# Kernel optimization log

Measured on AMD Instinct MI355X. Metric: run time of the kernel, lower is better.

The kernel has to match this reference:

```python
import jax, jax.numpy as jnp
import numpy as np

H = 1024      # hidden_dim
NH = 16       # num_heads
HD = H // NH  # head_dim
FFN = 4096
EPS = 1e-5


def setup_inputs() -> dict:
    key = jax.random.key(0)
    ks = jax.random.split(key, 12)
    s = 0.02
    return {
        "x": jax.random.normal(ks[0], (2, 2048, H), dtype=jnp.float32),
        "w_qkv": jax.random.normal(ks[1], (H, 3 * H), dtype=jnp.float32) * s,
        "b_qkv": jnp.zeros((3 * H,), dtype=jnp.float32),
        "w_out": jax.random.normal(ks[2], (H, H), dtype=jnp.float32) * s,
        "b_out": jnp.zeros((H,), dtype=jnp.float32),
        "ln1_g": jnp.ones((H,), dtype=jnp.float32),
        "ln1_b": jnp.zeros((H,), dtype=jnp.float32),
        "ln2_g": jnp.ones((H,), dtype=jnp.float32),
        "ln2_b": jnp.zeros((H,), dtype=jnp.float32),
        "w1": jax.random.normal(ks[3], (H, FFN), dtype=jnp.float32) * s,
        "b1": jnp.zeros((FFN,), dtype=jnp.float32),
        "w2": jax.random.normal(ks[4], (FFN, H), dtype=jnp.float32) * s,
        "b2": jnp.zeros((H,), dtype=jnp.float32),
    }


def _layernorm(x, g, b):
    mu = jnp.mean(x, axis=-1, keepdims=True)
    var = jnp.mean(jnp.square(x - mu), axis=-1, keepdims=True)
    return (x - mu) * jax.lax.rsqrt(var + EPS) * g + b


def reference(x, w_qkv, b_qkv, w_out, b_out, ln1_g, ln1_b, ln2_g, ln2_b, w1, b1, w2, b2):
    B, S, _ = x.shape
    # pre-LN attention branch
    h = _layernorm(x, ln1_g, ln1_b)
    qkv = h @ w_qkv + b_qkv                       # (B,S,3H)
    qkv = qkv.reshape(B, S, 3, NH, HD).transpose(2, 0, 3, 1, 4)
    q, k, v = qkv[0], qkv[1], qkv[2]              # (B,NH,S,HD)
    scores = jnp.einsum("bhqd,bhkd->bhqk", q, k) / jnp.sqrt(jnp.float32(HD))
    causal = jnp.triu(jnp.ones((S, S), dtype=bool), k=1)
    scores = jnp.where(causal, -jnp.inf, scores)
    attn = jax.nn.softmax(scores, axis=-1)
    out = jnp.einsum("bhqk,bhkd->bhqd", attn, v)  # (B,NH,S,HD)
    out = out.transpose(0, 2, 1, 3).reshape(B, S, H)
    attn_out = out @ w_out + b_out
    x = x + attn_out
    # FFN branch
    h2 = _layernorm(x, ln2_g, ln2_b)
    ffn = jax.nn.gelu(h2 @ w1 + b1, approximate=False) @ w2 + b2
    return x + ffn
```

## Files before the change

kernel.cpp:

```cpp
#include <hip/hip_runtime.h>
#include <hip/hip_bf16.h>

typedef __bf16 bf16_t;
typedef __bf16 bf16x8 __attribute__((ext_vector_type(8)));
typedef __bf16 bf16x4 __attribute__((ext_vector_type(4)));
typedef __bf16 bf16x2 __attribute__((ext_vector_type(2)));
typedef float  f32x4  __attribute__((ext_vector_type(4)));

#define HDIM 1024
#define SEQ  2048
#define NHEAD 16
#define HEADD 64

__device__ __forceinline__ void gld_lds16(const void* g, void* l) {
  __builtin_amdgcn_global_load_lds(
      (const __attribute__((address_space(1))) unsigned int*)g,
      (__attribute__((address_space(3))) unsigned int*)l, 16, 0, 0);
}

__global__ __launch_bounds__(256) void ln_kernel(const float* __restrict__ x,
                                                 const float* __restrict__ gam,
                                                 const float* __restrict__ bet,
                                                 bf16_t* __restrict__ out) {
  int row = blockIdx.x;
  int t = threadIdx.x;
  const float4* xr = (const float4*)(x + (size_t)row * HDIM);
  float4 v = xr[t];
  float s = v.x + v.y + v.z + v.w;
  float ss = v.x*v.x + v.y*v.y + v.z*v.z + v.w*v.w;
  #pragma unroll
  for (int o = 32; o > 0; o >>= 1) {
    s  += __shfl_xor(s, o);
    ss += __shfl_xor(ss, o);
  }
  __shared__ float red[8];
  int w = t >> 6;
  if ((t & 63) == 0) { red[w*2] = s; red[w*2+1] = ss; }
  __syncthreads();
  s  = red[0] + red[2] + red[4] + red[6];
  ss = red[1] + red[3] + red[5] + red[7];
  float mu  = s * (1.0f / HDIM);
  float var = ss * (1.0f / HDIM) - mu * mu;
  float rstd = rsqrtf(var + 1e-5f);
  float4 g4 = ((const float4*)gam)[t];
  float4 b4 = ((const float4*)bet)[t];
  bf16x4 o4;
  o4[0] = (bf16_t)((v.x - mu) * rstd * g4.x + b4.x);
  o4[1] = (bf16_t)((v.y - mu) * rstd * g4.y + b4.y);
  o4[2] = (bf16_t)((v.z - mu) * rstd * g4.z + b4.z);
  o4[3] = (bf16_t)((v.w - mu) * rstd * g4.w + b4.w);
  *(bf16x4*)(out + (size_t)row * HDIM + t * 4) = o4;
}

__global__ __launch_bounds__(256) void transpose_cast(const float* __restrict__ W,
                                                      bf16_t* __restrict__ Wt,
                                                      int Kd, int Nd) {
  __shared__ float tile[32][33];
  int n0 = blockIdx.x * 32, k0 = blockIdx.y * 32;
  int tx = threadIdx.x & 31, ty = threadIdx.x >> 5;
  #pragma unroll
  for (int i = 0; i < 4; i++)
    tile[ty + i*8][tx] = W[(size_t)(k0 + ty + i*8) * Nd + n0 + tx];
  __syncthreads();
  #pragma unroll
  for (int i = 0; i < 4; i++)
    Wt[(size_t)(n0 + ty + i*8) * Kd + k0 + tx] = (bf16_t)tile[tx][ty + i*8];
}

__device__ __forceinline__ float gelu_fast(float x) {
  float y = 0.7978845608f * (x + 0.044715f * x * x * x);
  float u = exp2f(y * 2.885390082f);
  float th = 1.0f - 2.0f * __builtin_amdgcn_rcpf(u + 1.0f);
  return 0.5f * x * (1.0f + th);
}

template<int EPI, int BN, int BK>
__global__ __launch_bounds__(256, 2)
void gemm_bt(const bf16_t* __restrict__ A, const bf16_t* __restrict__ Bt,
             const float* __restrict__ bias, const float* __restrict__ resid,
             void* __restrict__ outp, int M, int N, int K) {
  constexpr int NFRAG = BN / 32;
  constexpr int CH  = BK / 8;
  constexpr int SWZ = CH - 1;
  constexpr int RPP = 256 / CH;
  __shared__ bf16_t As[2][128*BK];
  __shared__ bf16_t Bs[2][BN*BK];
  int t = threadIdx.x;
  int w = t >> 6, l = t & 63;
  int wr = w >> 1, wc = w & 1;

  int nbx = gridDim.x;
  int bid = blockIdx.y * nbx + blockIdx.x;
  int chunkx = (nbx * gridDim.y) >> 3;
  int nb = (bid & 7) * chunkx + (bid >> 3);
  int bm = nb / nbx, bn = nb % nbx;
  size_t m0 = (size_t)bm * 128, n0 = (size_t)bn * BN;

  f32x4 acc[4][NFRAG];
  #pragma unroll
  for (int m = 0; m < 4; m++)
    #pragma unroll
    for (int n = 0; n < NFRAG; n++) acc[m][n] = (f32x4)(0.0f);

  int srow = t / CH;
  int scol = ((t & SWZ) ^ (srow & SWZ)) * 8;
  int dsto = t * 8;
  const bf16_t* ag = A  + (m0 + srow) * K + scol;
  const bf16_t* bg = Bt + (n0 + srow) * K + scol;

  int lr = l & 15, lg = l >> 4;

  auto stage = [&](int buf, int k0) {
    #pragma unroll
    for (int p = 0; p < 128/RPP; p++)
      gld_lds16(ag + k0 + (size_t)(p*RPP)*K, &As[buf][dsto + p*RPP*BK]);
    #pragma unroll
    for (int p = 0; p < BN/RPP; p++)
      gld_lds16(bg + k0 + (size_t)(p*RPP)*K, &Bs[buf][dsto + p*RPP*BK]);
  };

  stage(0, 0);
  __syncthreads();
  int cur = 0;
  for (int k0 = 0; k0 < K; k0 += BK) {
    if (k0 + BK < K) stage(cur ^ 1, k0 + BK);
    #pragma unroll
    for (int kk = 0; kk < BK/32; kk++) {
      bf16x8 af[4], bfr[NFRAG];
      #pragma unroll
      for (int m = 0; m < 4; m++) {
        int row = wr*64 + m*16 + lr;
        int off = row*BK*2 + (((kk*4 + lg) ^ (row & SWZ)) << 4);
        af[m] = *(const bf16x8*)((const char*)&As[cur][0] + off);
      }
      #pragma unroll
      for (int n = 0; n < NFRAG; n++) {
        int row = wc*(BN/2) + n*16 + lr;
        int off = row*BK*2 + (((kk*4 + lg) ^ (row & SWZ)) << 4);
        bfr[n] = *(const bf16x8*)((const char*)&Bs[cur][0] + off);
      }
      #pragma unroll
      for (int m = 0; m < 4; m++)
        #pragma unroll
        for (int n = 0; n < NFRAG; n++)
          acc[m][n] = __builtin_amdgcn_mfma_f32_16x16x32_bf16(af[m], bfr[n], acc[m][n], 0, 0, 0);
    }
    __syncthreads();
    cur ^= 1;
  }

  int r0 = (l >> 4) * 4, c0 = l & 15;
  #pragma unroll
  for (int m = 0; m < 4; m++) {
    #pragma unroll
    for (int n = 0; n < NFRAG; n++) {
      size_t row = m0 + wr*64 + m*16 + r0;
      size_t col = n0 + wc*(BN/2) + n*16 + c0;
      float bv = bias[col];
      #pragma unroll
      for (int r = 0; r < 4; r++) {
        float vv = acc[m][n][r] + bv;
        size_t idx = (row + r) * (size_t)N + col;
        if (EPI == 0) {
          ((bf16_t*)outp)[idx] = (bf16_t)vv;
        } else if (EPI == 1) {
          ((float*)outp)[idx] = vv + resid[idx];
        } else {
          ((bf16_t*)outp)[idx] = (bf16_t)gelu_fast(vv);
        }
      }
    }
  }
}

__global__ __launch_bounds__(512, 4)
void attn_kernel(const bf16_t* __restrict__ qkv, bf16_t* __restrict__ out) {
  int idx = blockIdx.x;
  int half = idx >> 8;
  int sub = idx & 255;
  int qth = sub >> 5;
  int qt = half ? qth : (15 - qth);
  int bh = sub & 31;
  int b = bh >> 4, h = bh & 15;
  int t = threadIdx.x, w = t >> 6, l = t & 63;

  __shared__ bf16_t Ks[2][64*64];
  __shared__ bf16_t Vt[2][64*72];
  __shared__ bf16_t Ps[8][16*64];

  const size_t RS = 3 * HDIM;
  const bf16_t* qb = qkv + (size_t)b * SEQ * RS + h * HEADD;
  const bf16_t* kb = qb + HDIM;
  const bf16_t* vb = qb + 2 * HDIM;

  int lr = l & 15, lg = l >> 4;
  const float SCALE = 0.125f * 1.44269504f;

  bf16x8 qf[2];
  {
    size_t qrow = (size_t)qt * 128 + w * 16 + lr;
    qf[0] = *(const bf16x8*)(qb + qrow * RS + lg * 8);
    qf[1] = *(const bf16x8*)(qb + qrow * RS + 32 + lg * 8);
    #pragma unroll
    for (int i = 0; i < 8; i++) {
      qf[0][i] = (bf16_t)((float)qf[0][i] * SCALE);
      qf[1][i] = (bf16_t)((float)qf[1][i] * SCALE);
    }
  }

  f32x4 o[4];
  #pragma unroll
  for (int d = 0; d < 4; d++) o[d] = (f32x4)(0.0f);
  float m = -1e30f, lsum = 0.0f;

  int srow = t >> 3, scol = (t & 7) * 8;
  int Fv = ((scol >> 3) & 7) << 3;
  int nkt = 2 * qt + 2;

  const bf16_t* kg0 = kb + (size_t)srow * RS + scol;
  const bf16_t* vg0 = vb + (size_t)srow * RS + scol;

  bf16x8 kr = *(const bf16x8*)kg0;
  bf16x8 vr = *(const bf16x8*)vg0;

  int wrow0 = qt * 128 + w * 16;
  int qg = wrow0 + lr;
  bf16_t* pw = Ps[w];
  int psw = (lr & 7) << 4;
  int cur = 0;

  for (int kt = 0; kt < nkt; kt++) {
    {
      int ba = srow * 128 + scol * 2;
      int sw = (srow & 7) << 4;
      *(bf16x8*)((char*)Ks[cur] + (ba ^ sw)) = kr;
      int ksw = srow ^ Fv;
      bf16_t* vt = Vt[cur];
      #pragma unroll
      for (int i = 0; i < 8; i++)
        vt[(scol + i) * 72 + ksw] = vr[i];
    }
    if (kt + 1 < nkt) {
      kr = *(const bf16x8*)(kg0 + (size_t)(kt + 1) * 64 * RS);
      vr = *(const bf16x8*)(vg0 + (size_t)(kt + 1) * 64 * RS);
    }
    __syncthreads();

    bool skipw = (kt * 64) > (wrow0 + 15);
    if (!skipw) {
      f32x4 sc[4];
      #pragma unroll
      for (int kt2 = 0; kt2 < 4; kt2++) {
        sc[kt2] = (f32x4)(0.0f);
        #pragma unroll
        for (int kk = 0; kk < 2; kk++) {
          int row = kt2 * 16 + lr;
          int off = (row * 128 + kk * 64 + lg * 16) ^ ((row & 7) << 4);
          bf16x8 kf = *(const bf16x8*)((char*)Ks[cur] + off);
          sc[kt2] = __builtin_amdgcn_mfma_f32_16x16x32_bf16(kf, qf[kk], sc[kt2], 0, 0, 0);
        }
      }
      if (kt * 64 + 63 > wrow0) {
        #pragma unroll
        for (int kt2 = 0; kt2 < 4; kt2++) {
          #pragma unroll
          for (int r = 0; r < 4; r++) {
            int kcol = kt*64 + kt2*16 + lg*4 + r;
            if (kcol > qg) sc[kt2][r] = -1e30f;
          }
        }
      }
      float tm0 = fmaxf(fmaxf(sc[0][0], sc[0][1]), fmaxf(sc[0][2], sc[0][3]));
      float tm1 = fmaxf(fmaxf(sc[1][0], sc[1][1]), fmaxf(sc[1][2], sc[1][3]));
      float tm2 = fmaxf(fmaxf(sc[2][0], sc[2][1]), fmaxf(sc[2][2], sc[2][3]));
      float tm3 = fmaxf(fmaxf(sc[3][0], sc[3][1]), fmaxf(sc[3][2], sc[3][3]));
      float tm = fmaxf(fmaxf(tm0, tm1), fmaxf(tm2, tm3));
      tm = fmaxf(tm, __shfl_xor(tm, 16));
      tm = fmaxf(tm, __shfl_xor(tm, 32));
      if (!__all(tm <= m + 8.0f)) {
        float nm = fmaxf(m, tm);
        float alpha = exp2f(m - nm);
        m = nm;
        lsum *= alpha;
        #pragma unroll
        for (int d = 0; d < 4; d++)
          #pragma unroll
          for (int r = 0; r < 4; r++) o[d][r] *= alpha;
      }
      #pragma unroll
      for (int kt2 = 0; kt2 < 4; kt2++) {
        float p0 = exp2f(sc[kt2][0] - m);
        float p1 = exp2f(sc[kt2][1] - m);
        float p2 = exp2f(sc[kt2][2] - m);
        float p3 = exp2f(sc[kt2][3] - m);
        lsum += (p0 + p1) + (p2 + p3);
        bf16x2 pa; pa[0] = (bf16_t)p0; pa[1] = (bf16_t)p1;
        bf16x2 pb; pb[0] = (bf16_t)p2; pb[1] = (bf16_t)p3;
        int base = lr * 128 + kt2 * 32 + lg * 8;
        *(bf16x2*)((char*)pw + ((base)     ^ psw)) = pa;
        *(bf16x2*)((char*)pw + ((base + 4) ^ psw)) = pb;
      }
      asm volatile("s_waitcnt lgkmcnt(0)" ::: "memory");
      #pragma unroll
      for (int kk = 0; kk < 2; kk++) {
        int poff = (lr * 128 + kk * 64 + lg * 16) ^ psw;
        bf16x8 pf = *(const bf16x8*)((char*)pw + poff);
        #pragma unroll
        for (int dblk = 0; dblk < 4; dblk++) {
          int vrow = dblk * 16 + lr;
          int Fd = ((vrow >> 3) & 7) << 3;
          bf16x8 vf = *(const bf16x8*)(Vt[cur] + vrow * 72 + ((kk * 32 + lg * 8) ^ Fd));
          o[dblk] = __builtin_amdgcn_mfma_f32_16x16x32_bf16(vf, pf, o[dblk], 0, 0, 0);
        }
      }
    }
    cur ^= 1;
  }

  lsum += __shfl_xor(lsum, 16);
  lsum += __shfl_xor(lsum, 32);
  float inv = 1.0f / lsum;

  bf16_t* ob = out + ((size_t)b * SEQ + qg) * HDIM + h * HEADD;
  #pragma unroll
  for (int dblk = 0; dblk < 4; dblk++) {
    bf16x4 q4;
    #pragma unroll
    for (int r = 0; r < 4; r++) q4[r] = (bf16_t)(o[dblk][r] * inv);
    *(bf16x4*)(ob + dblk * 16 + lg * 4) = q4;
  }
}

extern "C" void kernel_launch(void* const* d_in, const int* in_sizes, int n_in,
                              void* d_out, int out_size, void* d_ws, size_t ws_size,
                              hipStream_t stream) {
  (void)in_sizes; (void)n_in; (void)out_size; (void)ws_size;
  const float* x     = (const float*)d_in[0];
  const float* w_qkv = (const float*)d_in[1];
  const float* b_qkv = (const float*)d_in[2];
  const float* w_out = (const float*)d_in[3];
  const float* b_out = (const float*)d_in[4];
  const float* ln1_g = (const float*)d_in[5];
  const float* ln1_b = (const float*)d_in[6];
  const float* ln2_g = (const float*)d_in[7];
  const float* ln2_b = (const float*)d_in[8];
  const float* w1    = (const float*)d_in[9];
  const float* b1    = (const float*)d_in[10];
  const float* w2    = (const float*)d_in[11];
  const float* b2    = (const float*)d_in[12];
  float* out = (float*)d_out;

  char* ws = (char*)d_ws;
  size_t off = 0;
  auto alloc = [&](size_t bytes) -> void* {
    void* p = ws + off;
    off += (bytes + 255) & ~(size_t)255;
    return p;
  };
  bf16_t* wqkvT = (bf16_t*)alloc((size_t)3072*1024*2);
  bf16_t* woutT = (bf16_t*)alloc((size_t)1024*1024*2);
  bf16_t* w1T   = (bf16_t*)alloc((size_t)4096*1024*2);
  bf16_t* w2T   = (bf16_t*)alloc((size_t)1024*4096*2);
  bf16_t* ln1o  = (bf16_t*)alloc((size_t)4096*1024*2);
  bf16_t* qkvb  = (bf16_t*)alloc((size_t)4096*4096*2);
  bf16_t* attno = (bf16_t*)alloc((size_t)4096*1024*2);
  float*  x2    = (float*) alloc((size_t)4096*1024*4);
  bf16_t* h2 = ln1o;
  bf16_t* g  = qkvb;

  dim3 blk(256);
  transpose_cast<<<dim3(3072/32, 1024/32), blk, 0, stream>>>(w_qkv, wqkvT, 1024, 3072);
  transpose_cast<<<dim3(1024/32, 1024/32), blk, 0, stream>>>(w_out, woutT, 1024, 1024);
  transpose_cast<<<dim3(4096/32, 1024/32), blk, 0, stream>>>(w1,    w1T,   1024, 4096);
  transpose_cast<<<dim3(1024/32, 4096/32), blk, 0, stream>>>(w2,    w2T,   4096, 1024);

  ln_kernel<<<4096, blk, 0, stream>>>(x, ln1_g, ln1_b, ln1o);
  gemm_bt<0,128,32><<<dim3(24, 32), blk, 0, stream>>>(ln1o, wqkvT, b_qkv, nullptr, qkvb, 4096, 3072, 1024);
  attn_kernel<<<512, dim3(512), 0, stream>>>(qkvb, attno);
  gemm_bt<1,64,64><<<dim3(16, 32), blk, 0, stream>>>(attno, woutT, b_out, x, x2, 4096, 1024, 1024);
  ln_kernel<<<4096, blk, 0, stream>>>(x2, ln2_g, ln2_b, h2);
  gemm_bt<2,128,32><<<dim3(32, 32), blk, 0, stream>>>(h2, w1T, b1, nullptr, g, 4096, 4096, 1024);
  gemm_bt<1,64,64><<<dim3(16, 32), blk, 0, stream>>>(g, w2T, b2, x2, out, 4096, 1024, 4096);
}
```

Before: 236.1 us.

## Triple-buffer GEMM LDS staging with vmcnt waits and one barrier per k-step

Moves the bf16 GEMM from double to triple buffering in LDS. Loads are issued two k-steps ahead, and each step waits with explicit s_waitcnt vmcnt counts and a single barrier instead of two __syncthreads. For BK=32 it also changes the XOR swizzle to use row>>1, which should cut LDS bank conflicts, and it raises the occupancy hint to 3 for the BN=128 GEMMs. Together these should hide global-load latency better and remove a barrier per iteration, at the cost of more LDS per block and fragile hand-counted waitcnt values.

Result: slower. 243.7 us (+3.2%).

```diff
diff --git a/kernel.cpp b/kernel.cpp
--- a/kernel.cpp
+++ b/kernel.cpp
@@ -74,17 +74,21 @@
   return 0.5f * x * (1.0f + th);
 }
 
-template<int EPI, int BN, int BK>
-__global__ __launch_bounds__(256, 2)
+template<int EPI, int BN, int BK, int WPEU>
+__global__ __launch_bounds__(256, WPEU)
 void gemm_bt(const bf16_t* __restrict__ A, const bf16_t* __restrict__ Bt,
              const float* __restrict__ bias, const float* __restrict__ resid,
              void* __restrict__ outp, int M, int N, int K) {
   constexpr int NFRAG = BN / 32;
   constexpr int CH  = BK / 8;
   constexpr int SWZ = CH - 1;
+  constexpr int RSH = (BK == 32) ? 1 : 0;
   constexpr int RPP = 256 / CH;
-  __shared__ bf16_t As[2][128*BK];
-  __shared__ bf16_t Bs[2][BN*BK];
+  constexpr int APASS = 128 / RPP;
+  constexpr int BPASS = BN / RPP;
+  constexpr int L = APASS + BPASS;
+  __shared__ bf16_t As[3][128*BK];
+  __shared__ bf16_t Bs[3][BN*BK];
   int t = threadIdx.x;
   int w = t >> 6, l = t & 63;
   int wr = w >> 1, wc = w & 1;
@@ -103,7 +107,7 @@
     for (int n = 0; n < NFRAG; n++) acc[m][n] = (f32x4)(0.0f);
 
   int srow = t / CH;
-  int scol = ((t & SWZ) ^ (srow & SWZ)) * 8;
+  int scol = ((t & SWZ) ^ ((srow >> RSH) & SWZ)) * 8;
   int dsto = t * 8;
   const bf16_t* ag = A  + (m0 + srow) * K + scol;
   const bf16_t* bg = Bt + (n0 + srow) * K + scol;
@@ -112,31 +116,43 @@
 
   auto stage = [&](int buf, int k0) {
     #pragma unroll
-    for (int p = 0; p < 128/RPP; p++)
+    for (int p = 0; p < APASS; p++)
       gld_lds16(ag + k0 + (size_t)(p*RPP)*K, &As[buf][dsto + p*RPP*BK]);
     #pragma unroll
-    for (int p = 0; p < BN/RPP; p++)
+    for (int p = 0; p < BPASS; p++)
       gld_lds16(bg + k0 + (size_t)(p*RPP)*K, &Bs[buf][dsto + p*RPP*BK]);
   };
 
+  const int NK = K / BK;
   stage(0, 0);
-  __syncthreads();
+  stage(1, BK);
   int cur = 0;
-  for (int k0 = 0; k0 < K; k0 += BK) {
-    if (k0 + BK < K) stage(cur ^ 1, k0 + BK);
+  for (int k = 0; k < NK; k++) {
+    if (k < NK - 1) {
+      if constexpr (L == 4) asm volatile("s_waitcnt vmcnt(4)" ::: "memory");
+      else                  asm volatile("s_waitcnt vmcnt(6)" ::: "memory");
+    } else {
+      asm volatile("s_waitcnt vmcnt(0)" ::: "memory");
+    }
+    __builtin_amdgcn_s_barrier();
+    __builtin_amdgcn_sched_barrier(0);
+    if (k + 2 < NK) {
+      int nb3 = cur + 2; if (nb3 >= 3) nb3 -= 3;
+      stage(nb3, (k + 2) * BK);
+    }
     #pragma unroll
     for (int kk = 0; kk < BK/32; kk++) {
       bf16x8 af[4], bfr[NFRAG];
       #pragma unroll
       for (int m = 0; m < 4; m++) {
         int row = wr*64 + m*16 + lr;
-        int off = row*BK*2 + (((kk*4 + lg) ^ (row & SWZ)) << 4);
+        int off = row*BK*2 + (((kk*4 + lg) ^ ((row >> RSH) & SWZ)) << 4);
         af[m] = *(const bf16x8*)((const char*)&As[cur][0] + off);
       }
       #pragma unroll
       for (int n = 0; n < NFRAG; n++) {
         int row = wc*(BN/2) + n*16 + lr;
-        int off = row*BK*2 + (((kk*4 + lg) ^ (row & SWZ)) << 4);
+        int off = row*BK*2 + (((kk*4 + lg) ^ ((row >> RSH) & SWZ)) << 4);
         bfr[n] = *(const bf16x8*)((const char*)&Bs[cur][0] + off);
       }
       #pragma unroll
@@ -145,8 +161,7 @@
         for (int n = 0; n < NFRAG; n++)
           acc[m][n] = __builtin_amdgcn_mfma_f32_16x16x32_bf16(af[m], bfr[n], acc[m][n], 0, 0, 0);
     }
-    __syncthreads();
-    cur ^= 1;
+    cur = (cur == 2) ? 0 : cur + 1;
   }
 
   int r0 = (l >> 4) * 4, c0 = l & 15;
@@ -375,10 +390,10 @@
   transpose_cast<<<dim3(1024/32, 4096/32), blk, 0, stream>>>(w2,    w2T,   4096, 1024);
 
   ln_kernel<<<4096, blk, 0, stream>>>(x, ln1_g, ln1_b, ln1o);
-  gemm_bt<0,128,32><<<dim3(24, 32), blk, 0, stream>>>(ln1o, wqkvT, b_qkv, nullptr, qkvb, 4096, 3072, 1024);
+  gemm_bt<0,128,32,3><<<dim3(24, 32), blk, 0, stream>>>(ln1o, wqkvT, b_qkv, nullptr, qkvb, 4096, 3072, 1024);
   attn_kernel<<<512, dim3(512), 0, stream>>>(qkvb, attno);
-  gemm_bt<1,64,64><<<dim3(16, 32), blk, 0, stream>>>(attno, woutT, b_out, x, x2, 4096, 1024, 1024);
+  gemm_bt<1,64,64,2><<<dim3(16, 32), blk, 0, stream>>>(attno, woutT, b_out, x, x2, 4096, 1024, 1024);
   ln_kernel<<<4096, blk, 0, stream>>>(x2, ln2_g, ln2_b, h2);
-  gemm_bt<2,128,32><<<dim3(32, 32), blk, 0, stream>>>(h2, w1T, b1, nullptr, g, 4096, 4096, 1024);
-  gemm_bt<1,64,64><<<dim3(16, 32), blk, 0, stream>>>(g, w2T, b2, x2, out, 4096, 1024, 4096);
-}
+  gemm_bt<2,128,32,3><<<dim3(32, 32), blk, 0, stream>>>(h2, w1T, b1, nullptr, g, 4096, 4096, 1024);
+  gemm_bt<1,64,64,2><<<dim3(16, 32), blk, 0, stream>>>(g, w2T, b2, x2, out, 4096, 1024, 4096);
+}
```
